# Performance work log

Hardware: AMD Instinct MI355X
Metric: run time of the kernel (lower is better)

## Reference

```python
import jax, jax.numpy as jnp
import numpy as np

WS = (8, 7, 7)      # init window_size
SS = (4, 3, 3)      # init shift_size
HEADS = 4
EPS = 1e-3          # keras LayerNormalization default epsilon


def get_window_size(x_size, window_size, shift_size):
    ws = list(window_size); ss = list(shift_size)
    for i in range(len(x_size)):
        if x_size[i] <= window_size[i]:
            ws[i] = x_size[i]; ss[i] = 0
    return tuple(ws), tuple(ss)


def rel_pos_index(wd, wh, ww):
    # Faithful copy of get_relative_position_index (incl. its meshgrid quirks).
    y_y, z_z, x_x = np.meshgrid(np.arange(ww), np.arange(wd), np.arange(wh))  # indexing='xy'
    coords = np.stack([z_z, y_y, x_x], 0).reshape(3, -1)
    rel = (coords[:, :, None] - coords[:, None, :]).transpose(1, 2, 0)
    z = (rel[:, :, 0] + wd - 1) * (2 * wh - 1) * (2 * ww - 1)
    x = (rel[:, :, 1] + wh - 1) * (2 * ww - 1)
    y = rel[:, :, 2] + ww - 1
    return z + x + y  # (N, N) int


def window_partition(x, ws):
    B, D, H, W, C = x.shape
    x = x.reshape(B, D // ws[0], ws[0], H // ws[1], ws[1], W // ws[2], ws[2], C)
    x = x.transpose(0, 1, 3, 5, 2, 4, 6, 7)
    return x.reshape(-1, ws[0] * ws[1] * ws[2], C)


def window_reverse(w, ws, B, D, H, W):
    x = w.reshape(B, D // ws[0], H // ws[1], W // ws[2], ws[0], ws[1], ws[2], -1)
    x = x.transpose(0, 1, 4, 2, 5, 3, 6, 7)
    return x.reshape(B, D, H, W, -1)


def _slices(L, w, s):
    return [slice(0, -w), slice(-w, -s), slice(-s, None)] if s > 0 else [slice(None)]


def compute_mask(D, H, W, ws, ss):
    img = np.zeros((1, D, H, W, 1), np.float32)
    cnt = 0
    for d in _slices(D, ws[0], ss[0]):
        for h in _slices(H, ws[1], ss[1]):
            for w in _slices(W, ws[2], ss[2]):
                img[:, d, h, w, :] = cnt; cnt += 1
    x = img.reshape(1, D // ws[0], ws[0], H // ws[1], ws[1], W // ws[2], ws[2], 1)
    mw = x.transpose(0, 1, 3, 5, 2, 4, 6, 7).reshape(-1, ws[0] * ws[1] * ws[2])
    am = mw[:, None, :] - mw[:, :, None]
    return jnp.asarray(np.where(am != 0, -100.0, 0.0).astype(np.float32))  # (nW, N, N)


def layernorm(x, g, b):
    m = jnp.mean(x, -1, keepdims=True)
    v = jnp.mean(jnp.square(x - m), -1, keepdims=True)
    return (x - m) * jax.lax.rsqrt(v + EPS) * g + b


def setup_inputs() -> dict:
    key = jax.random.key(0)
    ks = jax.random.split(key, 8)
    C = 128; Hd = 4 * C
    f = lambda k, sh: jax.random.normal(k, sh, jnp.float32) * 0.02
    tbl = (2 * WS[0] - 1) * (2 * WS[1] - 1) * (2 * WS[2] - 1)
    return dict(
        x=jax.random.normal(ks[0], (2, 8, 56, 56, C), jnp.float32),
        norm1_g=jnp.ones((C,), jnp.float32), norm1_b=jnp.zeros((C,), jnp.float32),
        qkv_w=f(ks[1], (C, 3 * C)), qkv_b=jnp.zeros((3 * C,), jnp.float32),
        proj_w=f(ks[2], (C, C)), proj_b=jnp.zeros((C,), jnp.float32),
        rpb=f(ks[3], (tbl, HEADS)),
        norm2_g=jnp.ones((C,), jnp.float32), norm2_b=jnp.zeros((C,), jnp.float32),
        fc1_w=f(ks[4], (C, Hd)), fc1_b=jnp.zeros((Hd,), jnp.float32),
        fc2_w=f(ks[5], (Hd, C)), fc2_b=jnp.zeros((C,), jnp.float32),
    )


def reference(x, norm1_g, norm1_b, qkv_w, qkv_b, proj_w, proj_b, rpb,
              norm2_g, norm2_b, fc1_w, fc1_b, fc2_w, fc2_b):
    B, D, H, W, C = x.shape
    ws, ss = get_window_size((D, H, W), WS, SS)
    shortcut = x
    xn = layernorm(x, norm1_g, norm1_b)
    # dims divisible by window -> no padding branch
    shifted = jnp.roll(xn, (-ss[0], -ss[1], -ss[2]), (1, 2, 3)) if any(ss) else xn
    mask = compute_mask(D, H, W, ws, ss) if any(ss) else None

    xw = window_partition(shifted, ws)          # (B*nW, N, C)
    Bn, N, _ = xw.shape
    hd = C // HEADS
    scale = hd ** -0.5

    qkv = (xw @ qkv_w + qkv_b).reshape(Bn, N, 3, HEADS, hd).transpose(2, 0, 3, 1, 4)
    q, k, v = qkv[0] * scale, qkv[1], qkv[2]    # (Bn, heads, N, hd)
    attn = jnp.einsum('bhnd,bhmd->bhnm', q, k)
    idx = rel_pos_index(*WS)[:N, :N]
    bias = rpb[idx].transpose(2, 0, 1)          # (heads, N, N)
    attn = attn + bias[None]
    if mask is not None:
        nW = mask.shape[0]
        attn = attn.reshape(Bn // nW, nW, HEADS, N, N) + mask[None, :, None]
        attn = attn.reshape(-1, HEADS, N, N)
    attn = jax.nn.softmax(attn, axis=-1)
    out = jnp.einsum('bhnm,bhmd->bhnd', attn, v).transpose(0, 2, 1, 3).reshape(Bn, N, C)
    out = out @ proj_w + proj_b

    xr = window_reverse(out, ws, B, D, H, W)
    if any(ss):
        xr = jnp.roll(xr, ss, (1, 2, 3))
    x = shortcut + xr

    xn2 = layernorm(x, norm2_g, norm2_b)
    h = jax.nn.gelu(xn2 @ fc1_w + fc1_b, approximate=False)
    return x + (h @ fc2_w + fc2_b)
```

## Files before the change

kernel.cpp:

```cpp
#include <hip/hip_runtime.h>
#include <math.h>

#define TOK    50176
#define CH     128
#define NWIN   128
#define NTOK   392
#define NHEADS 4
#define QSCALE 0.17677669529663687f
#define LNEPS  1e-3f

typedef unsigned short u16;
typedef u16   u16x4  __attribute__((ext_vector_type(4)));
typedef u16   u16x8  __attribute__((ext_vector_type(8)));
typedef short s16x8  __attribute__((ext_vector_type(8)));
typedef float f32x4  __attribute__((ext_vector_type(4)));

__device__ __forceinline__ float bf2f(u16 u) {
    return __uint_as_float(((unsigned)u) << 16);
}
__device__ __forceinline__ u16 f2bf(float f) {
    unsigned u = __float_as_uint(f);
    return (u16)((u + 0x7fffu + ((u >> 16) & 1u)) >> 16);
}
__device__ __forceinline__ f32x4 mfma16(s16x8 a, s16x8 b, f32x4 c) {
    return __builtin_amdgcn_mfma_f32_16x16x32_bf16(a, b, c, 0, 0, 0);
}

__device__ __forceinline__ int src_index(int m) {
    int b = m / NTOK, t = m - b * NTOK;
    int batch = b >> 6, wIdx = b & 63;
    int bh = wIdx >> 3, bw = wIdx & 7;
    int d = t / 49, rem = t - d * 49;
    int h7 = rem / 7, w7 = rem - h7 * 7;
    int h = bh * 7 + h7 + 3; if (h >= 56) h -= 56;
    int w = bw * 7 + w7 + 3; if (w >= 56) w -= 56;
    return ((batch * 8 + d) * 56 + h) * 56 + w;
}

__global__ __launch_bounds__(256) void convT(
    const float* __restrict__ src, u16* __restrict__ dst,
    int K, int N, int scaleN)
{
    __shared__ float t[32][33];
    int n0 = blockIdx.x * 32, k0 = blockIdx.y * 32;
    int tx = threadIdx.x & 31, ty = threadIdx.x >> 5;
    #pragma unroll
    for (int r = 0; r < 4; ++r)
        t[ty + r * 8][tx] = src[(size_t)(k0 + ty + r * 8) * N + n0 + tx];
    __syncthreads();
    #pragma unroll
    for (int r = 0; r < 4; ++r) {
        int n = n0 + ty + r * 8;
        float sc = (n < scaleN) ? QSCALE : 1.f;
        dst[(size_t)n * K + k0 + tx] = f2bf(t[tx][ty + r * 8] * sc);
    }
}

__global__ __launch_bounds__(128) void ln_kernel(
    const float* __restrict__ xin,
    const float* __restrict__ g, const float* __restrict__ bta,
    u16* __restrict__ out)
{
    int m = blockIdx.x, c = threadIdx.x;
    float v = xin[(size_t)src_index(m) * CH + c];
    float s1 = v, s2 = v * v;
    #pragma unroll
    for (int o = 32; o; o >>= 1) { s1 += __shfl_xor(s1, o); s2 += __shfl_xor(s2, o); }
    __shared__ float ps[2][2];
    int w = c >> 6;
    if ((c & 63) == 0) { ps[w][0] = s1; ps[w][1] = s2; }
    __syncthreads();
    s1 = ps[0][0] + ps[1][0];
    s2 = ps[0][1] + ps[1][1];
    float mean = s1 * (1.f / CH);
    float var  = s2 * (1.f / CH) - mean * mean;
    float r = rsqrtf(var + LNEPS);
    out[(size_t)m * CH + c] = f2bf((v - mean) * r * g[c] + bta[c]);
}

template<int EPI, int KTOT>
__global__ __launch_bounds__(512, 6) void gemm_mfma(
    const u16* __restrict__ A, const u16* __restrict__ W,
    const float* __restrict__ bias, void* __restrict__ outp,
    int Nn, const float* __restrict__ resid,
    const float* __restrict__ lng, const float* __restrict__ lnb,
    u16* __restrict__ ln_out)
{
    __shared__ u16 As[4][64][32];
    __shared__ u16 Bs[4][128][32];
    __shared__ float lnred[2][4][16][2];

    int tid = threadIdx.x, w = tid >> 6, l = tid & 63;
    int c16 = l & 15, g4 = l >> 4;
    int m0 = blockIdx.y * 64, n0 = blockIdx.x * 128;
    int wm = w & 3, wn = w >> 2;
    const int NCH = KTOT / 128;

    f32x4 acc[4] = {};
    u16x8 va[2], vb[4];

    #pragma unroll
    for (int p = 0; p < 2; ++p) {
        int e = tid + p * 512, row = e >> 4, c8 = e & 15;
        va[p] = *(const u16x8*)&A[(size_t)(m0 + row) * KTOT + c8 * 8];
    }
    #pragma unroll
    for (int p = 0; p < 4; ++p) {
        int e = tid + p * 512, row = e >> 4, c8 = e & 15;
        vb[p] = *(const u16x8*)&W[(size_t)(n0 + row) * KTOT + c8 * 8];
    }
    for (int ch = 0; ch < NCH; ++ch) {
        #pragma unroll
        for (int p = 0; p < 2; ++p) {
            int e = tid + p * 512, row = e >> 4, c8 = e & 15;
            *(u16x8*)&As[c8 >> 2][row][(c8 & 3) * 8] = va[p];
        }
        #pragma unroll
        for (int p = 0; p < 4; ++p) {
            int e = tid + p * 512, row = e >> 4, c8 = e & 15;
            *(u16x8*)&Bs[c8 >> 2][row][(c8 & 3) * 8] = vb[p];
        }
        __syncthreads();
        if (ch + 1 < NCH) {
            #pragma unroll
            for (int p = 0; p < 2; ++p) {
                int e = tid + p * 512, row = e >> 4, c8 = e & 15;
                va[p] = *(const u16x8*)&A[(size_t)(m0 + row) * KTOT + (ch + 1) * 128 + c8 * 8];
            }
            #pragma unroll
            for (int p = 0; p < 4; ++p) {
                int e = tid + p * 512, row = e >> 4, c8 = e & 15;
                vb[p] = *(const u16x8*)&W[(size_t)(n0 + row) * KTOT + (ch + 1) * 128 + c8 * 8];
            }
        }
        #pragma unroll
        for (int kc = 0; kc < 4; ++kc) {
            s16x8 af = __builtin_bit_cast(s16x8,
                *(const u16x8*)&As[kc][wm * 16 + c16][g4 * 8]);
            #pragma unroll
            for (int ni = 0; ni < 4; ++ni) {
                s16x8 bf = __builtin_bit_cast(s16x8,
                    *(const u16x8*)&Bs[kc][wn * 64 + ni * 16 + c16][g4 * 8]);
                acc[ni] = mfma16(af, bf, acc[ni]);
            }
        }
        if (ch + 1 < NCH) __syncthreads();
    }

    if (EPI == 2) {
        float psum[4], psq[4];
        int dstl[4];
        #pragma unroll
        for (int r = 0; r < 4; ++r) {
            int m = m0 + wm * 16 + g4 * 4 + r;
            int dst = src_index(m);
            dstl[r] = dst;
            float s = 0.f, q = 0.f;
            #pragma unroll
            for (int ni = 0; ni < 4; ++ni) {
                int col = wn * 64 + ni * 16 + c16;
                float v = acc[ni][r] + bias[col] + resid[(size_t)dst * CH + col];
                acc[ni][r] = v;
                s += v; q += v * v;
            }
            psum[r] = s; psq[r] = q;
        }
        #pragma unroll
        for (int o = 1; o <= 8; o <<= 1)
            #pragma unroll
            for (int r = 0; r < 4; ++r) {
                psum[r] += __shfl_xor(psum[r], o);
                psq[r]  += __shfl_xor(psq[r], o);
            }
        if (c16 == 0) {
            #pragma unroll
            for (int r = 0; r < 4; ++r) {
                int rl = g4 * 4 + r;
                lnred[wn][wm][rl][0] = psum[r];
                lnred[wn][wm][rl][1] = psq[r];
            }
        }
        __syncthreads();
        float gl[4], bl[4];
        #pragma unroll
        for (int ni = 0; ni < 4; ++ni) {
            int col = wn * 64 + ni * 16 + c16;
            gl[ni] = lng[col]; bl[ni] = lnb[col];
        }
        #pragma unroll
        for (int r = 0; r < 4; ++r) {
            int rl = g4 * 4 + r;
            float s = lnred[0][wm][rl][0] + lnred[1][wm][rl][0];
            float q = lnred[0][wm][rl][1] + lnred[1][wm][rl][1];
            float mean = s * (1.f / CH);
            float var  = q * (1.f / CH) - mean * mean;
            float rstd = rsqrtf(var + LNEPS);
            int dst = dstl[r];
            #pragma unroll
            for (int ni = 0; ni < 4; ++ni) {
                int col = wn * 64 + ni * 16 + c16;
                float v = acc[ni][r];
                ((float*)outp)[(size_t)dst * CH + col] = v;
                ln_out[(size_t)dst * CH + col] = f2bf((v - mean) * rstd * gl[ni] + bl[ni]);
            }
        }
    } else {
        #pragma unroll
        for (int r = 0; r < 4; ++r) {
            int m = m0 + wm * 16 + g4 * 4 + r;
            #pragma unroll
            for (int ni = 0; ni < 4; ++ni) {
                int col = n0 + wn * 64 + ni * 16 + c16;
                float v = acc[ni][r];
                if (EPI == 1) {
                    v += bias[col] * (col < 128 ? QSCALE : 1.f);
                    ((u16*)outp)[(size_t)m * Nn + col] = f2bf(v);
                } else if (EPI == 3) {
                    v += bias[col];
                    v = 0.5f * v * (1.f + erff(v * 0.70710678118654752f));
                    ((u16*)outp)[(size_t)m * Nn + col] = f2bf(v);
                } else {
                    v += bias[col];
                    ((float*)outp)[(size_t)m * CH + col] = v + resid[(size_t)m * CH + col];
                }
            }
        }
    }
}

__global__ __launch_bounds__(64) void bias_k(
    const float* __restrict__ rpb, float* __restrict__ biasT2)
{
    int nt = blockIdx.x;
    int t  = blockIdx.y;
    int hw = blockIdx.z;
    int l  = threadIdx.x;
    int head = hw >> 2, wt = hw & 3;
    int bh7 = wt >> 1, bw7 = wt & 1;
    int j = nt * 16 + (l & 15);
    int rb = t * 16 + (l >> 4) * 4;
    f32x4 outv;
    #pragma unroll
    for (int r = 0; r < 4; ++r) {
        int i = rb + r; if (i > NTOK - 1) i = NTOK - 1;
        float v;
        if (j >= NTOK) v = -100.f;
        else {
            int di = i / 49, ri = i - di * 49, hi = ri / 7, wi = ri - hi * 7;
            int dj = j / 49, rj = j - dj * 49, hj = rj / 7, wj = rj - hj * 7;
            int bidx = (di - dj + 7) * 169 + (hi - hj + 6) * 13 + (wi - wj + 6);
            v = rpb[bidx * NHEADS + head];
            int regi = (bh7 ? (hi < 4 ? 1 : 2) : 0) * 3 + (bw7 ? (wi < 4 ? 1 : 2) : 0);
            int regj = (bh7 ? (hj < 4 ? 1 : 2) : 0) * 3 + (bw7 ? (wj < 4 ? 1 : 2) : 0);
            if (regi != regj) v -= 100.f;
        }
        outv[r] = v;
    }
    *(f32x4*)&biasT2[((((size_t)hw * 25 + t) * 26 + nt) << 8) + (l << 2)] = outv;
}

__global__ __launch_bounds__(512, 4) void attn_mfma(
    const u16* __restrict__ Qb, const float* __restrict__ biasT2,
    u16* __restrict__ O)
{
    __shared__ u16 Vt[32][420];
    __shared__ u16 Pst[8][16][40];

    int bid = blockIdx.x;
    int win = bid >> 2, head = bid & 3;
    int tid = threadIdx.x, w = tid >> 6, l = tid & 63;
    int c16 = l & 15, g4 = l >> 4;

    const size_t qbase = (size_t)win * NTOK * 384;
    for (int e = tid; e < 1600; e += 512) {
        int j = e >> 2, d0 = (e & 3) * 8;
        u16x8 vv = {0, 0, 0, 0, 0, 0, 0, 0};
        if (j < NTOK)
            vv = *(const u16x8*)&Qb[qbase + (size_t)j * 384 + 256 + head * 32 + d0];
        #pragma unroll
        for (int i = 0; i < 8; ++i) Vt[d0 + i][j] = vv[i];
    }
    {
        int e = tid;
        if (e < 32 * 16) Vt[e >> 4][400 + (e & 15)] = 0;
    }
    __syncthreads();

    int wIdx = win & 63;
    int wt = (((wIdx >> 3) == 7) ? 2 : 0) + (((wIdx & 7) == 7) ? 1 : 0);
    const float* bt = biasT2 + (((size_t)(head * 4 + wt) * 25 * 26) << 8) + (l << 2);
    u16 (*myP)[40] = Pst[w];
    const u16* kroot = Qb + qbase + 128 + head * 32 + g4 * 8;

    for (int t = w; t < 25; t += 8) {
        int row0 = t * 16;
        int qr = row0 + c16; if (qr > NTOK - 1) qr = NTOK - 1;
        s16x8 afrag = __builtin_bit_cast(s16x8,
            *(const u16x8*)&Qb[qbase + (size_t)qr * 384 + head * 32 + g4 * 8]);
        const float* btt = bt + (((size_t)t * 26) << 8);

        float l4[4] = {0.f, 0.f, 0.f, 0.f};
        f32x4 oacc[2] = {{0.f,0.f,0.f,0.f},{0.f,0.f,0.f,0.f}};

        for (int jb = 0; jb < 13; ++jb) {
            f32x4 s[2];
            #pragma unroll
            for (int kk = 0; kk < 2; ++kk) {
                f32x4 cb = *(const f32x4*)(btt + (((size_t)(jb * 2 + kk)) << 8));
                int kr = jb * 32 + kk * 16 + c16;
                if (kr > NTOK - 1) kr = NTOK - 1;
                s16x8 bfrag = __builtin_bit_cast(s16x8,
                    *(const u16x8*)&kroot[(size_t)kr * 384]);
                s[kk] = mfma16(afrag, bfrag, cb);
            }
            #pragma unroll
            for (int kk = 0; kk < 2; ++kk)
                #pragma unroll
                for (int r = 0; r < 4; ++r) {
                    float p = exp2f(s[kk][r] * 1.44269504f);
                    l4[r] += p;
                    myP[g4 * 4 + r][kk * 16 + c16] = f2bf(p);
                }
            s16x8 pa = __builtin_bit_cast(s16x8, *(const u16x8*)&myP[c16][g4 * 8]);
            #pragma unroll
            for (int nd = 0; nd < 2; ++nd) {
                s16x8 vb = __builtin_bit_cast(s16x8,
                    *(const u16x8*)&Vt[nd * 16 + c16][jb * 32 + g4 * 8]);
                oacc[nd] = mfma16(pa, vb, oacc[nd]);
            }
        }

        #pragma unroll
        for (int r = 0; r < 4; ++r) {
            #pragma unroll
            for (int o = 1; o <= 8; o <<= 1)
                l4[r] += __shfl_xor(l4[r], o);
            l4[r] = 1.f / l4[r];
        }

        #pragma unroll
        for (int nd = 0; nd < 2; ++nd)
            #pragma unroll
            for (int r = 0; r < 4; ++r) {
                int qrow = row0 + g4 * 4 + r;
                if (qrow < NTOK)
                    O[((size_t)(win * NTOK + qrow)) * CH + head * 32 + nd * 16 + c16]
                        = f2bf(oacc[nd][r] * l4[r]);
            }
    }
}

extern "C" void kernel_launch(void* const* d_in, const int* in_sizes, int n_in,
                              void* d_out, int out_size, void* d_ws, size_t ws_size,
                              hipStream_t stream) {
    const float* x      = (const float*)d_in[0];
    const float* n1g    = (const float*)d_in[1];
    const float* n1b    = (const float*)d_in[2];
    const float* qkv_w  = (const float*)d_in[3];
    const float* qkv_b  = (const float*)d_in[4];
    const float* proj_w = (const float*)d_in[5];
    const float* proj_b = (const float*)d_in[6];
    const float* rpb    = (const float*)d_in[7];
    const float* n2g    = (const float*)d_in[8];
    const float* n2b    = (const float*)d_in[9];
    const float* fc1_w  = (const float*)d_in[10];
    const float* fc1_b  = (const float*)d_in[11];
    const float* fc2_w  = (const float*)d_in[12];
    const float* fc2_b  = (const float*)d_in[13];
    float* out = (float*)d_out;

    char* ws = (char*)d_ws;
    size_t off = 0;
    u16* A_bf  = (u16*)(ws + off);  off += (size_t)TOK * 128 * 2;
    u16* Qb_bf = (u16*)(ws + off);  off += (size_t)TOK * 384 * 2;
    u16* O_bf  = (u16*)(ws + off);  off += (size_t)TOK * 128 * 2;
    float* R   = (float*)(ws + off); off += (size_t)TOK * 128 * 4;
    u16* qkvT  = (u16*)(ws + off);  off += 384 * 128 * 2;
    u16* projT = (u16*)(ws + off);  off += 128 * 128 * 2;
    u16* fc1T  = (u16*)(ws + off);  off += 512 * 128 * 2;
    u16* fc2T  = (u16*)(ws + off);  off += 128 * 512 * 2;
    u16* H_bf  = Qb_bf;
    float* biasT2 = (float*)A_bf;

    hipLaunchKernelGGL(convT, dim3(384/32, 128/32), dim3(256), 0, stream, qkv_w,  qkvT, 128, 384, 128);
    hipLaunchKernelGGL(convT, dim3(128/32, 128/32), dim3(256), 0, stream, proj_w, projT, 128, 128, 0);
    hipLaunchKernelGGL(convT, dim3(512/32, 128/32), dim3(256), 0, stream, fc1_w,  fc1T, 128, 512, 0);
    hipLaunchKernelGGL(convT, dim3(128/32, 512/32), dim3(256), 0, stream, fc2_w,  fc2T, 512, 128, 0);
    hipLaunchKernelGGL(ln_kernel, dim3(TOK), dim3(128), 0, stream, x, n1g, n1b, A_bf);
    hipLaunchKernelGGL((gemm_mfma<1, 128>), dim3(3, TOK/64), dim3(512), 0, stream,
                       A_bf, qkvT, qkv_b, Qb_bf, 384, nullptr, nullptr, nullptr, nullptr);
    hipLaunchKernelGGL(bias_k, dim3(26, 25, 16), dim3(64), 0, stream, rpb, biasT2);
    hipLaunchKernelGGL(attn_mfma, dim3(NWIN * NHEADS), dim3(512), 0, stream,
                       Qb_bf, biasT2, O_bf);
    hipLaunchKernelGGL((gemm_mfma<2, 128>), dim3(1, TOK/64), dim3(512), 0, stream,
                       O_bf, projT, proj_b, R, 128, x, n2g, n2b, A_bf);
    hipLaunchKernelGGL((gemm_mfma<3, 128>), dim3(4, TOK/64), dim3(512), 0, stream,
                       A_bf, fc1T, fc1_b, H_bf, 512, nullptr, nullptr, nullptr, nullptr);
    hipLaunchKernelGGL((gemm_mfma<4, 512>), dim3(1, TOK/64), dim3(512), 0, stream,
                       H_bf, fc2T, fc2_b, out, 128, R, nullptr, nullptr, nullptr);
}
```

Before: 178.6 us.

## Fold log2e into Q scale and bias, swap QK^T operands, shuffle P in registers

Folds log2(e) into the Q weight/bias scaling and the precomputed bias table so the attention softmax calls exp2 directly, dropping a per-element multiply. The score MFMA now computes S^T (K as A operand) with the bias table transposed to match. P is repacked into the PV A-fragment through cross-lane shuffles and packed bf16 converts instead of a per-wave LDS round trip. Row sums are reduced with fewer shuffles. This adds shuffle and select work and uses inline asm for v_cvt_pk_bf16_f32.

```diff
diff --git a/kernel.cpp b/kernel.cpp
--- a/kernel.cpp
+++ b/kernel.cpp
@@ -7,20 +7,28 @@
 #define NTOK   392
 #define NHEADS 4
 #define QSCALE 0.17677669529663687f
+#define LOG2E  1.44269504f
 #define LNEPS  1e-3f
 
 typedef unsigned short u16;
+typedef unsigned int   u32;
 typedef u16   u16x4  __attribute__((ext_vector_type(4)));
 typedef u16   u16x8  __attribute__((ext_vector_type(8)));
+typedef u32   u32x4  __attribute__((ext_vector_type(4)));
 typedef short s16x8  __attribute__((ext_vector_type(8)));
 typedef float f32x4  __attribute__((ext_vector_type(4)));
 
 __device__ __forceinline__ float bf2f(u16 u) {
-    return __uint_as_float(((unsigned)u) << 16);
+    return __uint_as_float(((u32)u) << 16);
 }
 __device__ __forceinline__ u16 f2bf(float f) {
-    unsigned u = __float_as_uint(f);
+    u32 u = __float_as_uint(f);
     return (u16)((u + 0x7fffu + ((u >> 16) & 1u)) >> 16);
+}
+__device__ __forceinline__ u32 pkbf(float a, float b) {
+    u32 r;
+    asm("v_cvt_pk_bf16_f32 %0, %1, %2" : "=v"(r) : "v"(a), "v"(b));
+    return r;
 }
 __device__ __forceinline__ f32x4 mfma16(s16x8 a, s16x8 b, f32x4 c) {
     return __builtin_amdgcn_mfma_f32_16x16x32_bf16(a, b, c, 0, 0, 0);
@@ -39,7 +47,7 @@
 
 __global__ __launch_bounds__(256) void convT(
     const float* __restrict__ src, u16* __restrict__ dst,
-    int K, int N, int scaleN)
+    int K, int N, int scaleN, float scaleArg)
 {
     __shared__ float t[32][33];
     int n0 = blockIdx.x * 32, k0 = blockIdx.y * 32;
@@ -51,7 +59,7 @@
     #pragma unroll
     for (int r = 0; r < 4; ++r) {
         int n = n0 + ty + r * 8;
-        float sc = (n < scaleN) ? QSCALE : 1.f;
+        float sc = (n < scaleN) ? scaleArg : 1.f;
         dst[(size_t)n * K + k0 + tx] = f2bf(t[tx][ty + r * 8] * sc);
     }
 }
@@ -213,7 +221,7 @@
                 int col = n0 + wn * 64 + ni * 16 + c16;
                 float v = acc[ni][r];
                 if (EPI == 1) {
-                    v += bias[col] * (col < 128 ? QSCALE : 1.f);
+                    v += bias[col] * (col < 128 ? QSCALE * LOG2E : 1.f);
                     ((u16*)outp)[(size_t)m * Nn + col] = f2bf(v);
                 } else if (EPI == 3) {
                     v += bias[col];
@@ -237,12 +245,13 @@
     int l  = threadIdx.x;
     int head = hw >> 2, wt = hw & 3;
     int bh7 = wt >> 1, bw7 = wt & 1;
-    int j = nt * 16 + (l & 15);
-    int rb = t * 16 + (l >> 4) * 4;
+    int i = t * 16 + (l & 15);
+    if (i > NTOK - 1) i = NTOK - 1;
+    int kb = nt * 16 + (l >> 4) * 4;
     f32x4 outv;
     #pragma unroll
     for (int r = 0; r < 4; ++r) {
-        int i = rb + r; if (i > NTOK - 1) i = NTOK - 1;
+        int j = kb + r;
         float v;
         if (j >= NTOK) v = -100.f;
         else {
@@ -254,7 +263,7 @@
             int regj = (bh7 ? (hj < 4 ? 1 : 2) : 0) * 3 + (bw7 ? (wj < 4 ? 1 : 2) : 0);
             if (regi != regj) v -= 100.f;
         }
-        outv[r] = v;
+        outv[r] = v * LOG2E;
     }
     *(f32x4*)&biasT2[((((size_t)hw * 25 + t) * 26 + nt) << 8) + (l << 2)] = outv;
 }
@@ -264,7 +273,6 @@
     u16* __restrict__ O)
 {
     __shared__ u16 Vt[32][420];
-    __shared__ u16 Pst[8][16][40];
 
     int bid = blockIdx.x;
     int win = bid >> 2, head = bid & 3;
@@ -280,48 +288,53 @@
         #pragma unroll
         for (int i = 0; i < 8; ++i) Vt[d0 + i][j] = vv[i];
     }
-    {
-        int e = tid;
-        if (e < 32 * 16) Vt[e >> 4][400 + (e & 15)] = 0;
-    }
+    if (tid < 32 * 16) Vt[tid >> 4][400 + (tid & 15)] = 0;
     __syncthreads();
 
     int wIdx = win & 63;
     int wt = (((wIdx >> 3) == 7) ? 2 : 0) + (((wIdx & 7) == 7) ? 1 : 0);
     const float* bt = biasT2 + (((size_t)(head * 4 + wt) * 25 * 26) << 8) + (l << 2);
-    u16 (*myP)[40] = Pst[w];
     const u16* kroot = Qb + qbase + 128 + head * 32 + g4 * 8;
 
+    int srcA = c16 + ((g4 & 1) << 5);
+    int srcB = srcA + 16;
+    bool hi = g4 >= 2;
+
     for (int t = w; t < 25; t += 8) {
-        int row0 = t * 16;
-        int qr = row0 + c16; if (qr > NTOK - 1) qr = NTOK - 1;
-        s16x8 afrag = __builtin_bit_cast(s16x8,
+        int q0 = t * 16;
+        int qr = q0 + c16; if (qr > NTOK - 1) qr = NTOK - 1;
+        s16x8 qfrag = __builtin_bit_cast(s16x8,
             *(const u16x8*)&Qb[qbase + (size_t)qr * 384 + head * 32 + g4 * 8]);
         const float* btt = bt + (((size_t)t * 26) << 8);
 
-        float l4[4] = {0.f, 0.f, 0.f, 0.f};
+        float lsum = 0.f;
         f32x4 oacc[2] = {{0.f,0.f,0.f,0.f},{0.f,0.f,0.f,0.f}};
 
         for (int jb = 0; jb < 13; ++jb) {
-            f32x4 s[2];
-            #pragma unroll
-            for (int kk = 0; kk < 2; ++kk) {
-                f32x4 cb = *(const f32x4*)(btt + (((size_t)(jb * 2 + kk)) << 8));
-                int kr = jb * 32 + kk * 16 + c16;
-                if (kr > NTOK - 1) kr = NTOK - 1;
-                s16x8 bfrag = __builtin_bit_cast(s16x8,
-                    *(const u16x8*)&kroot[(size_t)kr * 384]);
-                s[kk] = mfma16(afrag, bfrag, cb);
-            }
-            #pragma unroll
-            for (int kk = 0; kk < 2; ++kk)
-                #pragma unroll
-                for (int r = 0; r < 4; ++r) {
-                    float p = exp2f(s[kk][r] * 1.44269504f);
-                    l4[r] += p;
-                    myP[g4 * 4 + r][kk * 16 + c16] = f2bf(p);
-                }
-            s16x8 pa = __builtin_bit_cast(s16x8, *(const u16x8*)&myP[c16][g4 * 8]);
+            f32x4 s0, s1;
+            {
+                f32x4 cb = *(const f32x4*)(btt + (((size_t)(jb * 2 + 0)) << 8));
+                int kr = jb * 32 + c16; if (kr > NTOK - 1) kr = NTOK - 1;
+                s16x8 kfrag = __builtin_bit_cast(s16x8, *(const u16x8*)&kroot[(size_t)kr * 384]);
+                s0 = mfma16(kfrag, qfrag, cb);
+            }
+            {
+                f32x4 cb = *(const f32x4*)(btt + (((size_t)(jb * 2 + 1)) << 8));
+                int kr = jb * 32 + 16 + c16; if (kr > NTOK - 1) kr = NTOK - 1;
+                s16x8 kfrag = __builtin_bit_cast(s16x8, *(const u16x8*)&kroot[(size_t)kr * 384]);
+                s1 = mfma16(kfrag, qfrag, cb);
+            }
+            float p0 = exp2f(s0[0]), p1 = exp2f(s0[1]), p2 = exp2f(s0[2]), p3 = exp2f(s0[3]);
+            float p4 = exp2f(s1[0]), p5 = exp2f(s1[1]), p6 = exp2f(s1[2]), p7 = exp2f(s1[3]);
+            lsum += ((p0 + p1) + (p2 + p3)) + ((p4 + p5) + (p6 + p7));
+            u32 w0 = pkbf(p0, p1), w1 = pkbf(p2, p3);
+            u32 w2 = pkbf(p4, p5), w3 = pkbf(p6, p7);
+            u32 A0 = __shfl(w0, srcA), A1 = __shfl(w1, srcA);
+            u32 A2 = __shfl(w2, srcA), A3 = __shfl(w3, srcA);
+            u32 B0 = __shfl(w0, srcB), B1 = __shfl(w1, srcB);
+            u32 B2 = __shfl(w2, srcB), B3 = __shfl(w3, srcB);
+            u32x4 pw = { hi ? A2 : A0, hi ? A3 : A1, hi ? B2 : B0, hi ? B3 : B1 };
+            s16x8 pa = __builtin_bit_cast(s16x8, pw);
             #pragma unroll
             for (int nd = 0; nd < 2; ++nd) {
                 s16x8 vb = __builtin_bit_cast(s16x8,
@@ -330,22 +343,21 @@
             }
         }
 
-        #pragma unroll
-        for (int r = 0; r < 4; ++r) {
-            #pragma unroll
-            for (int o = 1; o <= 8; o <<= 1)
-                l4[r] += __shfl_xor(l4[r], o);
-            l4[r] = 1.f / l4[r];
-        }
+        lsum += __shfl_xor(lsum, 16);
+        lsum += __shfl_xor(lsum, 32);
+        float linv = 1.f / lsum;
+        float rinv[4];
+        #pragma unroll
+        for (int r = 0; r < 4; ++r) rinv[r] = __shfl(linv, g4 * 4 + r);
 
         #pragma unroll
         for (int nd = 0; nd < 2; ++nd)
             #pragma unroll
             for (int r = 0; r < 4; ++r) {
-                int qrow = row0 + g4 * 4 + r;
+                int qrow = q0 + g4 * 4 + r;
                 if (qrow < NTOK)
                     O[((size_t)(win * NTOK + qrow)) * CH + head * 32 + nd * 16 + c16]
-                        = f2bf(oacc[nd][r] * l4[r]);
+                        = f2bf(oacc[nd][r] * rinv[r]);
             }
     }
 }
@@ -382,10 +394,14 @@
     u16* H_bf  = Qb_bf;
     float* biasT2 = (float*)A_bf;
 
-    hipLaunchKernelGGL(convT, dim3(384/32, 128/32), dim3(256), 0, stream, qkv_w,  qkvT, 128, 384, 128);
-    hipLaunchKernelGGL(convT, dim3(128/32, 128/32), dim3(256), 0, stream, proj_w, projT, 128, 128, 0);
-    hipLaunchKernelGGL(convT, dim3(512/32, 128/32), dim3(256), 0, stream, fc1_w,  fc1T, 128, 512, 0);
-    hipLaunchKernelGGL(convT, dim3(128/32, 512/32), dim3(256), 0, stream, fc2_w,  fc2T, 512, 128, 0);
+    hipLaunchKernelGGL(convT, dim3(384/32, 128/32), dim3(256), 0, stream,
+                       qkv_w,  qkvT, 128, 384, 128, QSCALE * LOG2E);
+    hipLaunchKernelGGL(convT, dim3(128/32, 128/32), dim3(256), 0, stream,
+                       proj_w, projT, 128, 128, 0, 1.f);
+    hipLaunchKernelGGL(convT, dim3(512/32, 128/32), dim3(256), 0, stream,
+                       fc1_w,  fc1T, 128, 512, 0, 1.f);
+    hipLaunchKernelGGL(convT, dim3(128/32, 512/32), dim3(256), 0, stream,
+                       fc2_w,  fc2T, 512, 128, 0, 1.f);
     hipLaunchKernelGGL(ln_kernel, dim3(TOK), dim3(128), 0, stream, x, n1g, n1b, A_bf);
     hipLaunchKernelGGL((gemm_mfma<1, 128>), dim3(3, TOK/64), dim3(512), 0, stream,
                        A_bf, qkvT, qkv_b, Qb_bf, 384, nullptr, nullptr, nullptr, nullptr);
```

New measurement: 181.4 us. About the same (+1.6%).
